# Optimization experiments

Hardware: AMD Instinct MI355X
Metric: run time of the kernel (lower is better)

## Reference

```python
import jax, jax.numpy as jnp
import numpy as np

B, SL, D, E, STEPS = 8, 1024, 128, 4, 5


def setup_inputs() -> dict:
    key = jax.random.key(0)
    ks = jax.random.split(key, 13)
    s = 0.02  # xavier-ish init scale
    return {
        "batchinput": jax.random.normal(ks[0], (B, SL, D), jnp.float32),
        # dense per-edge-type adjacency [B, sl, sl*E]; scaled so bmm output stays O(1)
        "batchgraphin": jax.random.uniform(ks[1], (B, SL, SL * E), jnp.float32) / SL,
        "batchgraphout": jax.random.uniform(ks[2], (B, SL, SL * E), jnp.float32) / SL,
        "W_in": jax.random.normal(ks[3], (E * D, E * D), jnp.float32) * s,
        "b_in": jnp.zeros((E * D,), jnp.float32),
        "W_out": jax.random.normal(ks[4], (E * D, E * D), jnp.float32) * s,
        "b_out": jnp.zeros((E * D,), jnp.float32),
        "W_r": jax.random.normal(ks[5], (D, 3 * D), jnp.float32) * s,
        "b_r": jnp.zeros((D,), jnp.float32),
        "W_z": jax.random.normal(ks[6], (D, 3 * D), jnp.float32) * s,
        "b_z": jnp.zeros((D,), jnp.float32),
        "W_t": jax.random.normal(ks[7], (D, 3 * D), jnp.float32) * s,
        "b_t": jnp.zeros((D,), jnp.float32),
    }


def reference(batchinput, batchgraphin, batchgraphout,
              W_in, b_in, W_out, b_out,
              W_r, b_r, W_z, b_z, W_t, b_t):
    out = batchinput  # [B, SL, D]
    for _ in range(STEPS):
        # tile node state across edge types: [B, SL, E*D]
        temp = jnp.broadcast_to(out[:, :, None, :], (B, SL, E, D)).reshape(B, SL, E * D)
        gi = (temp @ W_in.T + b_in).reshape(B, SL * E, D)
        gi = jnp.einsum('bse,bed->bsd', batchgraphin, gi)   # [B, SL, D]
        go = (temp @ W_out.T + b_out).reshape(B, SL * E, D)
        go = jnp.einsum('bse,bed->bsd', batchgraphout, go)  # [B, SL, D]
        # GRU-style gated update
        cat = jnp.concatenate([gi, go, out], axis=-1)       # [B, SL, 3D]
        r = jax.nn.sigmoid(cat @ W_r.T + b_r)
        z = jax.nn.sigmoid(cat @ W_z.T + b_z)
        h_hat = jnp.tanh(jnp.concatenate([gi, go, r * out], axis=-1) @ W_t.T + b_t)
        out = (1.0 - z) * out + z * h_hat
    return out
```

## Files before the change

### kernel.cpp

```cpp
#include <hip/hip_runtime.h>
#include <cstdint>
#include <cstddef>


typedef unsigned short u16;
typedef unsigned int u32;
typedef float f32x4 __attribute__((ext_vector_type(4)));
typedef short short8 __attribute__((ext_vector_type(8)));
typedef u16 u16x4 __attribute__((ext_vector_type(4)));
typedef u16 u16x8 __attribute__((ext_vector_type(8)));

__device__ __forceinline__ float b2f(u16 h) {
  union { u32 u; float f; } v; v.u = ((u32)h) << 16; return v.f;
}
__device__ __forceinline__ u16 f2bf(float f) {
  union { float f; u32 u; } v; v.f = f;
  u32 r = (v.u + 0x7fffu + ((v.u >> 16) & 1u)) >> 16;
  return (u16)r;
}
__device__ __forceinline__ float ldu(const void* p, size_t i, int flag) {
  return flag ? ((const float*)p)[i] : b2f(((const u16*)p)[i]);
}
__device__ __forceinline__ void gload_lds16(const void* g, void* l) {
  __builtin_amdgcn_global_load_lds((const __attribute__((address_space(1))) void*)g,
                                   (__attribute__((address_space(3))) void*)l,
                                   16, 0, 0);
}

__global__ void k_detect(const u16* g, int* flag) {
  __shared__ int bad;
  if (threadIdx.x == 0) bad = 0;
  __syncthreads();
  int any = 0;
  for (int i = threadIdx.x; i < 8192; i += 256) any |= (g[i] > 0x3B00);
  if (any) atomicOr(&bad, 1);
  __syncthreads();
  if (threadIdx.x == 0) *flag = bad;
}

__global__ void k_cvtf(const void* src, float* dst, int n, const int* flagp) {
  int i = blockIdx.x * 256 + threadIdx.x;
  if (i < n) dst[i] = ldu(src, i, *flagp);
}

__global__ void k_weff(const void* Win, const void* bin, const void* Wout, const void* bout,
                       float* weffT, float* biasf, const int* flagp) {
  int flag = *flagp;
  int idx = blockIdx.x * 256 + threadIdx.x;
  int j = idx >> 7, k = idx & 127;
  float s = 0.f;
  if (j < 512) {
#pragma unroll
    for (int e = 0; e < 4; e++) s += ldu(Win, (size_t)j * 512 + e * 128 + k, flag);
  } else {
#pragma unroll
    for (int e = 0; e < 4; e++) s += ldu(Wout, (size_t)(j - 512) * 512 + e * 128 + k, flag);
  }
  weffT[k * 1024 + j] = s;
  if (idx < 1024) biasf[idx] = (idx < 512) ? ldu(bin, idx, flag) : ldu(bout, idx - 512, flag);
}

__global__ void k_wt(const void* W, const void* bv, float* WT, float* bf, const int* flagp) {
  int flag = *flagp;
  int idx = blockIdx.x * 256 + threadIdx.x;
  int n = idx / 384, k = idx % 384;
  WT[k * 128 + n] = ldu(W, idx, flag);
  if (idx < 128) bf[idx] = ldu(bv, idx, flag);
}

__global__ __launch_bounds__(256, 2) void kg_pre(const float* __restrict__ weffT,
                                                 const float* __restrict__ biasf,
                                                 const float* __restrict__ outF,
                                                 u16* __restrict__ gpreT) {
  __shared__ __align__(16) float xs[32 * 128];
  int t = threadIdx.x;
  int gb = blockIdx.y, gate = gb >> 3, b = gb & 7;
  int s0 = blockIdx.x * 32;
  for (int idx = t; idx < 4096; idx += 256)
    xs[idx] = outF[(size_t)(b * 1024 + s0 + (idx >> 7)) * 128 + (idx & 127)];
  __syncthreads();
  int d = t & 127, sh = t >> 7;
  const float* wp = weffT + gate * 512 + d;
  const float* xp = xs + sh * 16 * 128;
  float acc[4][16] = {};
  for (int k = 0; k < 128; k++) {
    float w0 = wp[k * 1024];
    float w1 = wp[k * 1024 + 128];
    float w2 = wp[k * 1024 + 256];
    float w3 = wp[k * 1024 + 384];
#pragma unroll
    for (int si = 0; si < 16; si++) {
      float x = xp[si * 128 + k];
      acc[0][si] += x * w0; acc[1][si] += x * w1;
      acc[2][si] += x * w2; acc[3][si] += x * w3;
    }
  }
  float bj0 = biasf[gate * 512 + d],       bj1 = biasf[gate * 512 + 128 + d];
  float bj2 = biasf[gate * 512 + 256 + d], bj3 = biasf[gate * 512 + 384 + d];
  u16* op = gpreT + (((size_t)(gb * 128 + d)) << 12) + ((size_t)(s0 + sh * 16) << 2);
#pragma unroll
  for (int sp = 0; sp < 8; sp++) {
    u16x8 v;
#pragma unroll
    for (int hh = 0; hh < 2; hh++) {
      int si = sp * 2 + hh;
      v[hh * 4 + 0] = f2bf(acc[0][si] + bj0);
      v[hh * 4 + 1] = f2bf(acc[1][si] + bj1);
      v[hh * 4 + 2] = f2bf(acc[2][si] + bj2);
      v[hh * 4 + 3] = f2bf(acc[3][si] + bj3);
    }
    *(u16x8*)(op + sp * 8) = v;
  }
}

__global__ __launch_bounds__(256, 2) void kg_bmm(
    const void* __restrict__ gin, const void* __restrict__ gout,
    u16* __restrict__ gB, int useGB, int writeStep,
    const u16* __restrict__ gpreT,
    float* __restrict__ P,
    const int* __restrict__ flagp) {
  __shared__ __align__(16) u16 bufA[2][4096];
  __shared__ __align__(16) u16 bufB[2][8192];

  int t = threadIdx.x;
  int lin0 = blockIdx.x + (blockIdx.y << 4) + (blockIdx.z << 8);
  int lin = ((lin0 & 7) << 6) + (lin0 >> 3);
  int mb = lin & 15, gb = (lin >> 4) & 15, kh = lin >> 8;
  int gate = gb >> 3, b = gb & 7;
  int ms0 = mb << 6;
  int kbase = kh << 11;

  int flag = *flagp;
  int doWrite = useGB && flag && writeStep;
  int readGB  = useGB && flag && !writeStep;
  int srcBF = (flag == 0) || readGB;

  const void* Asrc;
  size_t abase;
  if (readGB) { Asrc = gB;               abase = (((size_t)(gb * 1024 + ms0)) << 12) + kbase; }
  else        { Asrc = gate ? gout : gin; abase = (((size_t)(b  * 1024 + ms0)) << 12) + kbase; }
  size_t gwbase = (((size_t)(gb * 1024 + ms0)) << 12) + kbase;

  int arow = t >> 4;
  int acolE = (t & 15) << 2;
  int acb = (t & 15) << 3;
  int aswz = (arow & 7) << 4;
  int lane = t & 63, w = t >> 6;
  int wm = w >> 1, wn = w & 1;
  int lr = lane & 15, lk = lane >> 4;
  int r0 = wm * 32 + lr;
  int c0 = wn * 64 + lr;
  int fswz = (lr & 7) << 4;

  f32x4 acc[2][4] = {};
  f32x4 af[4]; u16x4 ah[4];

  auto stageA_load = [&](int st) {
    size_t kk = abase + (size_t)st * 64;
    if (srcBF) {
      const u16* p = (const u16*)Asrc;
#pragma unroll
      for (int it = 0; it < 4; it++)
        ah[it] = *(const u16x4*)(p + kk + (size_t)(arow + it * 16) * 4096 + acolE);
    } else {
      const float* p = (const float*)Asrc;
#pragma unroll
      for (int it = 0; it < 4; it++) {
        const f32x4* a = (const f32x4*)(p + kk + (size_t)(arow + it * 16) * 4096 + acolE);
        af[it] = doWrite ? __builtin_nontemporal_load(a) : *a;
      }
    }
  };
  auto stageA_write = [&](int nb, int st) {
#pragma unroll
    for (int it = 0; it < 4; it++) {
      int row = arow + it * 16;
      u16x4 v;
      if (srcBF) v = ah[it];
      else { v[0] = f2bf(af[it][0]); v[1] = f2bf(af[it][1]);
             v[2] = f2bf(af[it][2]); v[3] = f2bf(af[it][3]); }
      *(u16x4*)((char*)bufA[nb] + row * 128 + (acb ^ aswz)) = v;
      if (doWrite)
        *(u16x4*)(gB + gwbase + (size_t)st * 64 + (size_t)row * 4096 + acolE) = v;
    }
  };
  auto stageB = [&](int st, int nb) {
    size_t kk = (size_t)kbase + (size_t)st * 64;
#pragma unroll
    for (int c = 0; c < 4; c++) {
      int col = (w << 5) + (c << 3) + (lane >> 3);
      int j = (lane & 7) ^ (col & 7);
      const u16* g = gpreT + (((size_t)(gb * 128 + col)) << 12) + kk + (size_t)j * 8;
      u16* l = &bufB[nb][w * 2048 + c * 512];
      gload_lds16(g, l);
    }
  };
  auto compute = [&](int cur) {
    const char* A = (const char*)bufA[cur];
    const char* B = (const char*)bufB[cur];
#pragma unroll
    for (int ks = 0; ks < 2; ks++) {
      int kb = (ks * 64 + lk * 16) ^ fswz;
      short8 a0 = *(const short8*)(A + r0 * 128 + kb);
      short8 a1 = *(const short8*)(A + r0 * 128 + 2048 + kb);
#pragma unroll
      for (int nf = 0; nf < 4; nf++) {
        short8 bv = *(const short8*)(B + c0 * 128 + nf * 2048 + kb);
        acc[0][nf] = __builtin_amdgcn_mfma_f32_16x16x32_bf16(a0, bv, acc[0][nf], 0, 0, 0);
        acc[1][nf] = __builtin_amdgcn_mfma_f32_16x16x32_bf16(a1, bv, acc[1][nf], 0, 0, 0);
      }
    }
  };

  stageA_load(0);
  stageB(0, 0);
  stageA_write(0, 0);
  __syncthreads();
  int cur = 0;
#pragma unroll 2
  for (int st = 0; st < 32; st++) {
    if (st < 31) { stageA_load(st + 1); stageB(st + 1, cur ^ 1); }
    compute(cur);
    if (st < 31) stageA_write(cur ^ 1, st + 1);
    __syncthreads();
    cur ^= 1;
  }

  float* Pp = P + (((size_t)(kh * 16 + gb)) << 17);
#pragma unroll
  for (int mf = 0; mf < 2; mf++) {
#pragma unroll
    for (int nf = 0; nf < 4; nf++) {
      int rowb = ms0 + wm * 32 + mf * 16 + lk * 4;
      int col = wn * 64 + nf * 16 + lr;
#pragma unroll
      for (int j = 0; j < 4; j++)
        Pp[(size_t)(rowb + j) * 128 + col] = acc[mf][nf][j];
    }
  }
}

__global__ __launch_bounds__(256, 2) void kg_gate(
    const float* __restrict__ P, float* __restrict__ outF,
    const float* __restrict__ WTr, const float* __restrict__ WTz,
    const float* __restrict__ WTt,
    const float* __restrict__ brf, const float* __restrict__ bzf,
    const float* __restrict__ btf,
    const int* __restrict__ flagp, void* __restrict__ dout, int writeOut) {
  __shared__ __align__(16) float cs[16 * 384];
  __shared__ __align__(16) float rs[16 * 128];
  int t = threadIdx.x;
  int m0 = blockIdx.x * 16;
  int b = m0 >> 10;
  for (int i4 = t; i4 < 1536; i4 += 256) {
    int r = i4 / 96, q = i4 % 96;
    int m = m0 + r, s = m & 1023;
    f32x4 v;
    if (q < 64) {
      int gate = q >> 5;
      size_t idx = (((size_t)(gate * 8 + b)) << 17) + ((size_t)s << 7) + ((size_t)(q & 31) << 2);
      v = *(const f32x4*)(P + idx) + *(const f32x4*)(P + ((size_t)1 << 21) + idx);
    } else {
      v = *(const f32x4*)(outF + ((size_t)m << 7) + ((q - 64) << 2));
    }
    *(f32x4*)&cs[r * 384 + (q << 2)] = v;
  }
  __syncthreads();
  int n = t & 127, mh = t >> 7;
  float accR[8] = {}, accZ[8] = {}, accT[8] = {};
  for (int kq = 0; kq < 64; kq++) {
    float wr[4], wz[4], wt[4];
#pragma unroll
    for (int kl = 0; kl < 4; kl++) {
      wr[kl] = WTr[(kq * 4 + kl) * 128 + n];
      wz[kl] = WTz[(kq * 4 + kl) * 128 + n];
      wt[kl] = WTt[(kq * 4 + kl) * 128 + n];
    }
#pragma unroll
    for (int mi = 0; mi < 8; mi++) {
      f32x4 c = *(const f32x4*)&cs[(mh * 8 + mi) * 384 + kq * 4];
#pragma unroll
      for (int kl = 0; kl < 4; kl++) {
        accR[mi] += c[kl] * wr[kl];
        accZ[mi] += c[kl] * wz[kl];
        accT[mi] += c[kl] * wt[kl];
      }
    }
  }
  for (int kq = 64; kq < 96; kq++) {
    float wr[4], wz[4];
#pragma unroll
    for (int kl = 0; kl < 4; kl++) {
      wr[kl] = WTr[(kq * 4 + kl) * 128 + n];
      wz[kl] = WTz[(kq * 4 + kl) * 128 + n];
    }
#pragma unroll
    for (int mi = 0; mi < 8; mi++) {
      f32x4 c = *(const f32x4*)&cs[(mh * 8 + mi) * 384 + kq * 4];
#pragma unroll
      for (int kl = 0; kl < 4; kl++) {
        accR[mi] += c[kl] * wr[kl];
        accZ[mi] += c[kl] * wz[kl];
      }
    }
  }
  float bR = brf[n], bZ = bzf[n], bT = btf[n];
  float z8[8];
#pragma unroll
  for (int mi = 0; mi < 8; mi++) {
    int row = mh * 8 + mi;
    float r = 1.f / (1.f + __expf(-(accR[mi] + bR)));
    z8[mi] = 1.f / (1.f + __expf(-(accZ[mi] + bZ)));
    rs[row * 128 + n] = r * cs[row * 384 + 256 + n];
  }
  __syncthreads();
  for (int kq = 0; kq < 32; kq++) {
    float wt[4];
#pragma unroll
    for (int kl = 0; kl < 4; kl++) wt[kl] = WTt[(256 + kq * 4 + kl) * 128 + n];
#pragma unroll
    for (int mi = 0; mi < 8; mi++) {
      f32x4 c = *(const f32x4*)&rs[(mh * 8 + mi) * 128 + kq * 4];
#pragma unroll
      for (int kl = 0; kl < 4; kl++) accT[mi] += c[kl] * wt[kl];
    }
  }
  int flag = *flagp;
#pragma unroll
  for (int mi = 0; mi < 8; mi++) {
    int row = mh * 8 + mi;
    int m = m0 + row;
    size_t o = (size_t)m * 128 + n;
    float h = tanhf(accT[mi] + bT);
    float z = z8[mi];
    float ov = cs[row * 384 + 256 + n];
    float res = (1.f - z) * ov + z * h;
    outF[o] = res;
    if (writeOut) {
      if (flag) ((float*)dout)[o] = res;
      else      ((u16*)dout)[o] = f2bf(res);
    }
  }
}

extern "C" void kernel_launch(void* const* d_in, const int* in_sizes, int n_in,
                              void* d_out, int out_size, void* d_ws, size_t ws_size,
                              hipStream_t stream) {
  const void* X    = d_in[0];
  const void* Gin  = d_in[1];
  const void* Gout = d_in[2];
  const void* Win  = d_in[3];
  const void* bin  = d_in[4];
  const void* Wout = d_in[5];
  const void* bout = d_in[6];
  const void* Wr   = d_in[7];
  const void* br   = d_in[8];
  const void* Wz   = d_in[9];
  const void* bz   = d_in[10];
  const void* Wt   = d_in[11];
  const void* bt   = d_in[12];

  char* w = (char*)d_ws;
  auto alloc = [&](size_t n) { char* p = w; w += (n + 255) & ~(size_t)255; return p; };
  int*   flag    = (int*)alloc(4);
  float* weffT   = (float*)alloc((size_t)128 * 1024 * 4);
  float* biasf   = (float*)alloc(1024 * 4);
  float* WTr     = (float*)alloc((size_t)384 * 128 * 4);
  float* WTz     = (float*)alloc((size_t)384 * 128 * 4);
  float* WTt     = (float*)alloc((size_t)384 * 128 * 4);
  float* brf     = (float*)alloc(128 * 4);
  float* bzf     = (float*)alloc(128 * 4);
  float* btf     = (float*)alloc(128 * 4);
  float* outF    = (float*)alloc((size_t)8192 * 128 * 4);
  u16*   gpreT   = (u16*)alloc((size_t)16 * 128 * 4096 * 2);
  float* partial = (float*)alloc((size_t)2 * 16 * 1024 * 128 * 4);
  u16*   gB      = (u16*)alloc((size_t)2 * 8 * 1024 * 4096 * 2);
  int wsok = ((size_t)(w - (char*)d_ws) <= ws_size) ? 1 : 0;
  (void)in_sizes; (void)n_in; (void)out_size;

  k_detect<<<1, 256, 0, stream>>>((const u16*)Gin, flag);
  k_weff<<<512, 256, 0, stream>>>(Win, bin, Wout, bout, weffT, biasf, flag);
  k_wt<<<192, 256, 0, stream>>>(Wr, br, WTr, brf, flag);
  k_wt<<<192, 256, 0, stream>>>(Wz, bz, WTz, bzf, flag);
  k_wt<<<192, 256, 0, stream>>>(Wt, bt, WTt, btf, flag);
  k_cvtf<<<4096, 256, 0, stream>>>(X, outF, 1048576, flag);

  for (int step = 0; step < 5; step++) {
    kg_pre<<<dim3(32, 16), 256, 0, stream>>>(weffT, biasf, outF, gpreT);
    kg_bmm<<<dim3(16, 16, 2), 256, 0, stream>>>(Gin, Gout, gB, wsok,
                                                (step == 0) ? 1 : 0,
                                                gpreT, partial, flag);
    kg_gate<<<512, 256, 0, stream>>>(partial, outF, WTr, WTz, WTt, brf, bzf, btf,
                                     flag, d_out, (step == 4) ? 1 : 0);
  }
}
```

Before: 1.048 ms.

## Move pre-projection GEMM to split-bf16 MFMA and template bmm A-load path

Replaces the scalar FP32 kg_pre with an MFMA kernel. It splits activations and weights into bf16 high and low parts and does three MFMAs per fragment to keep near-fp32 accuracy. The result is transposed through LDS into the gpreT layout. The bmm kernel is templated so later steps read the cached bf16 graph directly, and it converts fp32 at load time instead of holding fp32 registers across compute. The change trades extra MFMA work and a 64KB LDS staging buffer for far fewer scalar FMAs, and reduces register pressure in bmm.

```diff
diff --git a/kernel.cpp b/kernel.cpp
--- a/kernel.cpp
+++ b/kernel.cpp
@@ -44,7 +44,7 @@
 }
 
 __global__ void k_weff(const void* Win, const void* bin, const void* Wout, const void* bout,
-                       float* weffT, float* biasf, const int* flagp) {
+                       u16* weffHT, u16* weffLT, float* biasf, const int* flagp) {
   int flag = *flagp;
   int idx = blockIdx.x * 256 + threadIdx.x;
   int j = idx >> 7, k = idx & 127;
@@ -56,7 +56,9 @@
 #pragma unroll
     for (int e = 0; e < 4; e++) s += ldu(Wout, (size_t)(j - 512) * 512 + e * 128 + k, flag);
   }
-  weffT[k * 1024 + j] = s;
+  u16 h = f2bf(s);
+  weffHT[(size_t)j * 128 + k] = h;
+  weffLT[(size_t)j * 128 + k] = f2bf(s - b2f(h));
   if (idx < 1024) biasf[idx] = (idx < 512) ? ldu(bin, idx, flag) : ldu(bout, idx - 512, flag);
 }
 
@@ -68,51 +70,85 @@
   if (idx < 128) bf[idx] = ldu(bv, idx, flag);
 }
 
-__global__ __launch_bounds__(256, 2) void kg_pre(const float* __restrict__ weffT,
-                                                 const float* __restrict__ biasf,
-                                                 const float* __restrict__ outF,
-                                                 u16* __restrict__ gpreT) {
-  __shared__ __align__(16) float xs[32 * 128];
+__global__ __launch_bounds__(512, 2) void kg_pre_mfma(
+    const u16* __restrict__ weffHT, const u16* __restrict__ weffLT,
+    const float* __restrict__ biasf, const float* __restrict__ outF,
+    u16* __restrict__ gpreT) {
+  __shared__ __align__(16) u16 AH[32 * 128];
+  __shared__ __align__(16) u16 AL[32 * 128];
+  __shared__ __align__(16) u16 ybuf[32 * 1024];
   int t = threadIdx.x;
-  int gb = blockIdx.y, gate = gb >> 3, b = gb & 7;
+  int b = blockIdx.y;
   int s0 = blockIdx.x * 32;
-  for (int idx = t; idx < 4096; idx += 256)
-    xs[idx] = outF[(size_t)(b * 1024 + s0 + (idx >> 7)) * 128 + (idx & 127)];
-  __syncthreads();
-  int d = t & 127, sh = t >> 7;
-  const float* wp = weffT + gate * 512 + d;
-  const float* xp = xs + sh * 16 * 128;
-  float acc[4][16] = {};
-  for (int k = 0; k < 128; k++) {
-    float w0 = wp[k * 1024];
-    float w1 = wp[k * 1024 + 128];
-    float w2 = wp[k * 1024 + 256];
-    float w3 = wp[k * 1024 + 384];
-#pragma unroll
-    for (int si = 0; si < 16; si++) {
-      float x = xp[si * 128 + k];
-      acc[0][si] += x * w0; acc[1][si] += x * w1;
-      acc[2][si] += x * w2; acc[3][si] += x * w3;
-    }
-  }
-  float bj0 = biasf[gate * 512 + d],       bj1 = biasf[gate * 512 + 128 + d];
-  float bj2 = biasf[gate * 512 + 256 + d], bj3 = biasf[gate * 512 + 384 + d];
-  u16* op = gpreT + (((size_t)(gb * 128 + d)) << 12) + ((size_t)(s0 + sh * 16) << 2);
-#pragma unroll
-  for (int sp = 0; sp < 8; sp++) {
+  {
+    int row = t >> 4, c8 = (t & 15) * 8;
+    const float* src = outF + (((size_t)(b * 1024 + s0 + row)) << 7) + c8;
+    f32x4 x0 = *(const f32x4*)src;
+    f32x4 x1 = *(const f32x4*)(src + 4);
+    u16x8 vh, vl;
+#pragma unroll
+    for (int i = 0; i < 4; i++) {
+      float x = x0[i]; u16 h = f2bf(x);
+      vh[i] = h; vl[i] = f2bf(x - b2f(h));
+      x = x1[i]; h = f2bf(x);
+      vh[i + 4] = h; vl[i + 4] = f2bf(x - b2f(h));
+    }
+    int bc = (c8 * 2) ^ ((row & 7) << 4);
+    *(u16x8*)((char*)AH + row * 256 + bc) = vh;
+    *(u16x8*)((char*)AL + row * 256 + bc) = vl;
+  }
+  __syncthreads();
+  int lane = t & 63, w = t >> 6;
+  int wm = w >> 2, wn = w & 3;
+  int lr = lane & 15, lk = lane >> 4;
+  int n0 = wn * 256;
+  int arow = wm * 16 + lr;
+  int abase_row = arow * 256;
+  int aswz = (arow & 7) << 4;
+  f32x4 acc[16] = {};
+#pragma unroll
+  for (int kk = 0; kk < 4; kk++) {
+    int kb = (kk * 64 + lk * 16) ^ aswz;
+    short8 ah = *(const short8*)((const char*)AH + abase_row + kb);
+    short8 al = *(const short8*)((const char*)AL + abase_row + kb);
+    int wko = kk * 64 + lk * 16;
+#pragma unroll
+    for (int nf = 0; nf < 16; nf++) {
+      int j = n0 + nf * 16 + lr;
+      short8 wh = *(const short8*)((const char*)weffHT + (size_t)j * 256 + wko);
+      short8 wl = *(const short8*)((const char*)weffLT + (size_t)j * 256 + wko);
+      acc[nf] = __builtin_amdgcn_mfma_f32_16x16x32_bf16(ah, wh, acc[nf], 0, 0, 0);
+      acc[nf] = __builtin_amdgcn_mfma_f32_16x16x32_bf16(ah, wl, acc[nf], 0, 0, 0);
+      acc[nf] = __builtin_amdgcn_mfma_f32_16x16x32_bf16(al, wh, acc[nf], 0, 0, 0);
+    }
+  }
+#pragma unroll
+  for (int nf = 0; nf < 16; nf++) {
+    int j = n0 + nf * 16 + lr;
+    float bj = biasf[j];
+#pragma unroll
+    for (int i = 0; i < 4; i++) {
+      int s = wm * 16 + lk * 4 + i;
+      ybuf[s * 1024 + j] = f2bf(acc[nf][i] + bj);
+    }
+  }
+  __syncthreads();
+#pragma unroll
+  for (int p = 0; p < 8; p++) {
+    int row = p * 32 + (t >> 4);
+    int gate = row >> 7, d = row & 127;
+    int c = (t & 15) * 8;
     u16x8 v;
 #pragma unroll
-    for (int hh = 0; hh < 2; hh++) {
-      int si = sp * 2 + hh;
-      v[hh * 4 + 0] = f2bf(acc[0][si] + bj0);
-      v[hh * 4 + 1] = f2bf(acc[1][si] + bj1);
-      v[hh * 4 + 2] = f2bf(acc[2][si] + bj2);
-      v[hh * 4 + 3] = f2bf(acc[3][si] + bj3);
-    }
-    *(u16x8*)(op + sp * 8) = v;
-  }
-}
-
+    for (int i = 0; i < 8; i++) {
+      int k2 = c + i;
+      v[i] = ybuf[(k2 >> 2) * 1024 + gate * 512 + (k2 & 3) * 128 + d];
+    }
+    *(u16x8*)(gpreT + (((size_t)((gate * 8 + b) * 128 + d)) << 12) + (size_t)s0 * 4 + c) = v;
+  }
+}
+
+template <int WMODE>
 __global__ __launch_bounds__(256, 2) void kg_bmm(
     const void* __restrict__ gin, const void* __restrict__ gout,
     u16* __restrict__ gB, int useGB, int writeStep,
@@ -131,14 +167,18 @@
   int kbase = kh << 11;
 
   int flag = *flagp;
-  int doWrite = useGB && flag && writeStep;
-  int readGB  = useGB && flag && !writeStep;
-  int srcBF = (flag == 0) || readGB;
-
+  int doWrite = 0, srcBF = 1;
   const void* Asrc;
   size_t abase;
-  if (readGB) { Asrc = gB;               abase = (((size_t)(gb * 1024 + ms0)) << 12) + kbase; }
-  else        { Asrc = gate ? gout : gin; abase = (((size_t)(b  * 1024 + ms0)) << 12) + kbase; }
+  if (WMODE == 0) {
+    if (flag) { Asrc = gB;                abase = (((size_t)(gb * 1024 + ms0)) << 12) + kbase; }
+    else      { Asrc = gate ? gout : gin; abase = (((size_t)(b  * 1024 + ms0)) << 12) + kbase; }
+  } else {
+    doWrite = useGB && flag && writeStep;
+    srcBF = (flag == 0);
+    Asrc = gate ? gout : gin;
+    abase = (((size_t)(b * 1024 + ms0)) << 12) + kbase;
+  }
   size_t gwbase = (((size_t)(gb * 1024 + ms0)) << 12) + kbase;
 
   int arow = t >> 4;
@@ -153,11 +193,11 @@
   int fswz = (lr & 7) << 4;
 
   f32x4 acc[2][4] = {};
-  f32x4 af[4]; u16x4 ah[4];
+  u16x4 ah[4];
 
   auto stageA_load = [&](int st) {
     size_t kk = abase + (size_t)st * 64;
-    if (srcBF) {
+    if (WMODE == 0 || srcBF) {
       const u16* p = (const u16*)Asrc;
 #pragma unroll
       for (int it = 0; it < 4; it++)
@@ -167,22 +207,19 @@
 #pragma unroll
       for (int it = 0; it < 4; it++) {
         const f32x4* a = (const f32x4*)(p + kk + (size_t)(arow + it * 16) * 4096 + acolE);
-        af[it] = doWrite ? __builtin_nontemporal_load(a) : *a;
+        f32x4 af = doWrite ? __builtin_nontemporal_load(a) : *a;
+        u16x4 v;
+        v[0] = f2bf(af[0]); v[1] = f2bf(af[1]); v[2] = f2bf(af[2]); v[3] = f2bf(af[3]);
+        ah[it] = v;
+        if (doWrite)
+          *(u16x4*)(gB + gwbase + (size_t)st * 64 + (size_t)(arow + it * 16) * 4096 + acolE) = v;
       }
     }
   };
-  auto stageA_write = [&](int nb, int st) {
-#pragma unroll
-    for (int it = 0; it < 4; it++) {
-      int row = arow + it * 16;
-      u16x4 v;
-      if (srcBF) v = ah[it];
-      else { v[0] = f2bf(af[it][0]); v[1] = f2bf(af[it][1]);
-             v[2] = f2bf(af[it][2]); v[3] = f2bf(af[it][3]); }
-      *(u16x4*)((char*)bufA[nb] + row * 128 + (acb ^ aswz)) = v;
-      if (doWrite)
-        *(u16x4*)(gB + gwbase + (size_t)st * 64 + (size_t)row * 4096 + acolE) = v;
-    }
+  auto stageA_write = [&](int nb) {
+#pragma unroll
+    for (int it = 0; it < 4; it++)
+      *(u16x4*)((char*)bufA[nb] + (arow + it * 16) * 128 + (acb ^ aswz)) = ah[it];
   };
   auto stageB = [&](int st, int nb) {
     size_t kk = (size_t)kbase + (size_t)st * 64;
@@ -214,14 +251,14 @@
 
   stageA_load(0);
   stageB(0, 0);
-  stageA_write(0, 0);
+  stageA_write(0);
   __syncthreads();
   int cur = 0;
 #pragma unroll 2
   for (int st = 0; st < 32; st++) {
     if (st < 31) { stageA_load(st + 1); stageB(st + 1, cur ^ 1); }
     compute(cur);
-    if (st < 31) stageA_write(cur ^ 1, st + 1);
+    if (st < 31) stageA_write(cur ^ 1);
     __syncthreads();
     cur ^= 1;
   }
@@ -363,7 +400,8 @@
   char* w = (char*)d_ws;
   auto alloc = [&](size_t n) { char* p = w; w += (n + 255) & ~(size_t)255; return p; };
   int*   flag    = (int*)alloc(4);
-  float* weffT   = (float*)alloc((size_t)128 * 1024 * 4);
+  u16*   weffHT  = (u16*)alloc((size_t)1024 * 128 * 2);
+  u16*   weffLT  = (u16*)alloc((size_t)1024 * 128 * 2);
   float* biasf   = (float*)alloc(1024 * 4);
   float* WTr     = (float*)alloc((size_t)384 * 128 * 4);
   float* WTz     = (float*)alloc((size_t)384 * 128 * 4);
@@ -379,17 +417,21 @@
   (void)in_sizes; (void)n_in; (void)out_size;
 
   k_detect<<<1, 256, 0, stream>>>((const u16*)Gin, flag);
-  k_weff<<<512, 256, 0, stream>>>(Win, bin, Wout, bout, weffT, biasf, flag);
+  k_weff<<<512, 256, 0, stream>>>(Win, bin, Wout, bout, weffHT, weffLT, biasf, flag);
   k_wt<<<192, 256, 0, stream>>>(Wr, br, WTr, brf, flag);
   k_wt<<<192, 256, 0, stream>>>(Wz, bz, WTz, bzf, flag);
   k_wt<<<192, 256, 0, stream>>>(Wt, bt, WTt, btf, flag);
   k_cvtf<<<4096, 256, 0, stream>>>(X, outF, 1048576, flag);
 
   for (int step = 0; step < 5; step++) {
-    kg_pre<<<dim3(32, 16), 256, 0, stream>>>(weffT, biasf, outF, gpreT);
-    kg_bmm<<<dim3(16, 16, 2), 256, 0, stream>>>(Gin, Gout, gB, wsok,
-                                                (step == 0) ? 1 : 0,
-                                                gpreT, partial, flag);
+    kg_pre_mfma<<<dim3(32, 8), 512, 0, stream>>>(weffHT, weffLT, biasf, outF, gpreT);
+    if (step == 0 || !wsok)
+      kg_bmm<1><<<dim3(16, 16, 2), 256, 0, stream>>>(Gin, Gout, gB, wsok,
+                                                     (step == 0) ? 1 : 0,
+                                                     gpreT, partial, flag);
+    else
+      kg_bmm<0><<<dim3(16, 16, 2), 256, 0, stream>>>(Gin, Gout, gB, wsok, 0,
+                                                     gpreT, partial, flag);
     kg_gate<<<512, 256, 0, stream>>>(partial, outF, WTr, WTz, WTt, brf, bzf, btf,
                                      flag, d_out, (step == 4) ? 1 : 0);
   }
```

After: 1.057 ms. Within noise of the previous version (+0.8%).
